# Kernel tuning notes

Measured on AMD Instinct MI355X. Metric: run time of the kernel, lower is better.

The kernel has to match this reference:

```python
import jax, jax.numpy as jnp
import numpy as np

KSZ = 3      # kernel_size
NH = 4       # num_heads


def setup_inputs() -> dict:
    key = jax.random.key(0)
    ks = jax.random.split(key, 4)
    B, D, H, W, C = 1, 28, 28, 28, 192
    N = D * H * W
    s = 0.02  # trunc_normal std used by the module's init
    return {
        "x": jax.random.normal(ks[0], (B, N, C), jnp.float32),
        "Wq": jax.random.normal(ks[1], (C, C), jnp.float32) * s,
        "bq": jnp.zeros((C,), jnp.float32),
        "Wkv": jax.random.normal(ks[2], (C, 2 * C), jnp.float32) * s,
        "bkv": jnp.zeros((2 * C,), jnp.float32),
        "Wp": jax.random.normal(ks[3], (C, C), jnp.float32) * s,
        "bp": jnp.zeros((C,), jnp.float32),
        "D": D, "H": H, "W": W,
    }


def _windows(t, D, H, W):
    # t: (B, D+2, H+2, W+2, nh, hc) zero-padded; gather the 27 neighborhood
    # offsets (same flattening order as unfold: d-major, then h, then w).
    return jnp.stack(
        [t[:, dz:dz + D, dy:dy + H, dx:dx + W]
         for dz in range(KSZ) for dy in range(KSZ) for dx in range(KSZ)],
        axis=4)  # (B, D, H, W, 27, nh, hc)


def reference(x, Wq, bq, Wkv, bkv, Wp, bp, D, H, W):
    B, N, C = x.shape
    hc = C // NH
    scale = hc ** (-0.5)
    xv = x.reshape(B, D, H, W, C)

    q = (xv @ Wq + bq).reshape(B, D, H, W, NH, hc) * scale
    kv = (xv @ Wkv + bkv).reshape(B, D, H, W, 2, NH, hc)
    k, v = kv[..., 0, :, :], kv[..., 1, :, :]

    pad = ((0, 0), (1, 1), (1, 1), (1, 1), (0, 0), (0, 0))
    kwin = _windows(jnp.pad(k, pad), D, H, W)  # (B,D,H,W,27,nh,hc)
    vwin = _windows(jnp.pad(v, pad), D, H, W)

    # per-voxel 1x27 attention over the 3x3x3 neighborhood
    attn = jnp.einsum('bdhwnc,bdhwknc->bdhwnk', q, kwin)
    attn = jax.nn.softmax(attn, axis=-1)
    out = jnp.einsum('bdhwnk,bdhwknc->bdhwnc', attn, vwin)
    out = out.reshape(B, D, H, W, C) @ Wp + bp
    return out.reshape(B, N, C)
```

## Files before the change

### kernel.cpp

```cpp
#include <hip/hip_runtime.h>
#include <hip/hip_bf16.h>
#include <math.h>

#define CDIM 192
#define DD 28
#define NVOX (DD * DD * DD)
#define NLINE (DD * DD)
#define LSTRIDE (24 * DD * 8)

typedef __attribute__((ext_vector_type(8))) short bf16x8;
typedef __attribute__((ext_vector_type(4))) float f32x4;

__device__ __forceinline__ float blo(unsigned int u) {
  union { unsigned int i; float f; } w; w.i = u << 16; return w.f;
}
__device__ __forceinline__ float bhi(unsigned int u) {
  union { unsigned int i; float f; } w; w.i = u & 0xffff0000u; return w.f;
}
__device__ __forceinline__ unsigned short f2bf(float f) {
  union { float ff; unsigned int i; } w; w.ff = f;
  unsigned int x = w.i;
  return (unsigned short)((x + 0x7fffu + ((x >> 16) & 1u)) >> 16);
}
__device__ __forceinline__ unsigned int pk2(float lo, float hi) {
  __hip_bfloat162 h = __float22bfloat162_rn(make_float2(lo, hi));
  union { __hip_bfloat162 h2; unsigned int u; } cv; cv.h2 = h; return cv.u;
}

__global__ __launch_bounds__(256) void prep_w(
    const float* __restrict__ Wq, const float* __restrict__ Wkv,
    const float* __restrict__ Wp, const float* __restrict__ bq,
    const float* __restrict__ bkv,
    unsigned short* __restrict__ WqkvT, unsigned short* __restrict__ WpT,
    float* __restrict__ biasAll, float scale)
{
  int t = blockIdx.x * 256 + threadIdx.x;
  if (t < 576 * CDIM) {
    const int n = t / CDIM, k = t % CDIM;
    const float v = (n < CDIM) ? Wq[k * CDIM + n] * scale
                               : Wkv[k * 2 * CDIM + (n - CDIM)];
    WqkvT[t] = f2bf(v);
    return;
  }
  t -= 576 * CDIM;
  if (t < CDIM * CDIM) {
    const int n = t / CDIM, k = t % CDIM;
    WpT[t] = f2bf(Wp[k * CDIM + n]);
    return;
  }
  t -= CDIM * CDIM;
  if (t < 576)
    biasAll[t] = (t < CDIM) ? bq[t] * scale : bkv[t - CDIM];
}

__global__ __launch_bounds__(256) void gemm_qkv(
    const float* __restrict__ X,
    const unsigned short* __restrict__ Bt,
    const float* __restrict__ biasAll,
    unsigned short* __restrict__ qb,
    unsigned short* __restrict__ kxb,
    unsigned short* __restrict__ vxb)
{
  __shared__ unsigned short As[64 * 200];
  __shared__ unsigned short Bs[64 * 200];
  const int tid = threadIdx.x;
  const int m0 = blockIdx.x * 64;
  const int by = blockIdx.y;

#pragma unroll
  for (int u = tid; u < 1536; u += 256) {
    const int row = u / 24, c = (u % 24) * 8;
    const float4 f0 = *(const float4*)(&X[(size_t)(m0 + row) * CDIM + c]);
    const float4 f1 = *(const float4*)(&X[(size_t)(m0 + row) * CDIM + c + 4]);
    unsigned int o[4] = {pk2(f0.x, f0.y), pk2(f0.z, f0.w),
                         pk2(f1.x, f1.y), pk2(f1.z, f1.w)};
    *(uint4*)(&As[row * 200 + c]) = *(const uint4*)o;
  }

  const int l = tid & 63, w = tid >> 6;
  const int wm = (w >> 1) * 32, wn = (w & 1) * 32;
  const int lr = l & 15, lk = (l >> 4) * 8;
  const unsigned short* pa = &As[(wm + lr) * 200 + lk];
  const unsigned short* pb = &Bs[(wn + lr) * 200 + lk];

  for (int nt = by; nt < 9; nt += 3) {
    const int n0 = nt * 64;
    __syncthreads();
#pragma unroll
    for (int u = tid; u < 1536; u += 256) {
      const int row = u / 24, c = (u % 24) * 8;
      *(uint4*)(&Bs[row * 200 + c]) =
          *(const uint4*)(&Bt[(size_t)(n0 + row) * CDIM + c]);
    }
    __syncthreads();

    f32x4 acc[2][2] = {};
#pragma unroll
    for (int k0 = 0; k0 < CDIM; k0 += 32) {
      const bf16x8 a0 = *(const bf16x8*)(pa + k0);
      const bf16x8 a1 = *(const bf16x8*)(pa + 16 * 200 + k0);
      const bf16x8 b0 = *(const bf16x8*)(pb + k0);
      const bf16x8 b1 = *(const bf16x8*)(pb + 16 * 200 + k0);
      acc[0][0] = __builtin_amdgcn_mfma_f32_16x16x32_bf16(a0, b0, acc[0][0], 0, 0, 0);
      acc[0][1] = __builtin_amdgcn_mfma_f32_16x16x32_bf16(a0, b1, acc[0][1], 0, 0, 0);
      acc[1][0] = __builtin_amdgcn_mfma_f32_16x16x32_bf16(a1, b0, acc[1][0], 0, 0, 0);
      acc[1][1] = __builtin_amdgcn_mfma_f32_16x16x32_bf16(a1, b1, acc[1][1], 0, 0, 0);
    }

#pragma unroll
    for (int i = 0; i < 2; ++i)
#pragma unroll
      for (int j = 0; j < 2; ++j) {
        const int gc = n0 + wn + j * 16 + lr;
        const float bv = biasAll[gc];
#pragma unroll
        for (int r = 0; r < 4; ++r) {
          const int gr = m0 + wm + i * 16 + (l >> 4) * 4 + r;
          const float v = acc[i][j][r] + bv;
          const unsigned short bfv = f2bf(v);
          if (gc < CDIM) {
            qb[(size_t)gr * CDIM + gc] = bfv;
          } else {
            const int cc = (gc < 2 * CDIM) ? gc - CDIM : gc - 2 * CDIM;
            const int zy = gr / DD, xx = gr - zy * DD;
            const int dst = zy * LSTRIDE + (cc >> 3) * (DD * 8) + xx * 8 + (cc & 7);
            if (gc < 2 * CDIM) kxb[dst] = bfv;
            else               vxb[dst] = bfv;
          }
        }
      }
  }
}

__global__ __launch_bounds__(256, 3) void attn3d_xint(
    const unsigned short* __restrict__ q,
    const unsigned short* __restrict__ kx,
    const unsigned short* __restrict__ vx,
    unsigned short* __restrict__ y)
{
  const int bid = blockIdx.x;
  const int zy = (bid & 7) * 98 + (bid >> 3);
  const int z = zy / 28, yr = zy % 28;
  const int h = threadIdx.x >> 6;
  const int lane = threadIdx.x & 63;
  const int x = lane & 31;
  const int xc = x < 28 ? x : 27;
  const int g = lane >> 5;
  const int cb = h * 48 + g * 24;
  const int cgb = h * 6 + g * 3;
  const int vox = zy * 28 + xc;

  float qf[24];
  {
    const uint4* qp = (const uint4*)(q + (size_t)vox * CDIM + cb);
    const uint4 a = qp[0], b = qp[1], c = qp[2];
    const unsigned int uu[12] = {a.x, a.y, a.z, a.w, b.x, b.y, b.z, b.w,
                                 c.x, c.y, c.z, c.w};
#pragma unroll
    for (int i = 0; i < 12; ++i) { qf[2*i] = blo(uu[i]); qf[2*i+1] = bhi(uu[i]); }
  }

  const int nx = 3 - (x == 0) - (x == 27);
  const int ny = 3 - (yr == 0) - (yr == 27);
  const int nz = 3 - (z == 0) - (z == 27);
  const int noob = 27 - nx * ny * nz;
  float m = noob ? 0.f : -INFINITY;
  float s = (float)noob;
  float out[24];
#pragma unroll
  for (int i = 0; i < 24; ++i) out[i] = 0.f;

  const bool okm = (x > 0), okp = (x < 27);
  const int xm = okm ? xc - 1 : 0;
  const int xp = okp ? xc + 1 : 27;

  int offm[3], offc[3], offp[3];
#pragma unroll
  for (int i = 0; i < 3; ++i) {
    const int ub = (cgb + i) * (DD * 8);
    offm[i] = ub + xm * 8; offc[i] = ub + xc * 8; offp[i] = ub + xp * 8;
  }

  for (int dz = -1; dz <= 1; ++dz) {
    const int zz = z + dz;
    if ((unsigned)zz >= 28u) continue;
    for (int dy = -1; dy <= 1; ++dy) {
      const int yv = yr + dy;
      if ((unsigned)yv >= 28u) continue;
      const size_t lbase = (size_t)(zz * 28 + yv) * LSTRIDE;
      const unsigned short* kl = kx + lbase;
      const unsigned short* vl = vx + lbase;

      const uint4 Km0 = *(const uint4*)(kl + offm[0]);
      const uint4 Km1 = *(const uint4*)(kl + offm[1]);
      const uint4 Km2 = *(const uint4*)(kl + offm[2]);
      const uint4 Kc0 = *(const uint4*)(kl + offc[0]);
      const uint4 Kc1 = *(const uint4*)(kl + offc[1]);
      const uint4 Kc2 = *(const uint4*)(kl + offc[2]);
      const uint4 Kp0 = *(const uint4*)(kl + offp[0]);
      const uint4 Kp1 = *(const uint4*)(kl + offp[1]);
      const uint4 Kp2 = *(const uint4*)(kl + offp[2]);
      const unsigned int km[12] = {Km0.x, Km0.y, Km0.z, Km0.w, Km1.x, Km1.y,
                                   Km1.z, Km1.w, Km2.x, Km2.y, Km2.z, Km2.w};
      const unsigned int kc[12] = {Kc0.x, Kc0.y, Kc0.z, Kc0.w, Kc1.x, Kc1.y,
                                   Kc1.z, Kc1.w, Kc2.x, Kc2.y, Kc2.z, Kc2.w};
      const unsigned int kp[12] = {Kp0.x, Kp0.y, Kp0.z, Kp0.w, Kp1.x, Kp1.y,
                                   Kp1.z, Kp1.w, Kp2.x, Kp2.y, Kp2.z, Kp2.w};
      float p0 = 0.f, p1 = 0.f, p2 = 0.f;
#pragma unroll
      for (int i = 0; i < 12; ++i) {
        p0 += qf[2*i] * blo(km[i]) + qf[2*i+1] * bhi(km[i]);
        p1 += qf[2*i] * blo(kc[i]) + qf[2*i+1] * bhi(kc[i]);
        p2 += qf[2*i] * blo(kp[i]) + qf[2*i+1] * bhi(kp[i]);
      }
      p0 += __shfl_xor(p0, 32);
      p1 += __shfl_xor(p1, 32);
      p2 += __shfl_xor(p2, 32);

      const uint4 Vm0 = *(const uint4*)(vl + offm[0]);
      const uint4 Vm1 = *(const uint4*)(vl + offm[1]);
      const uint4 Vm2 = *(const uint4*)(vl + offm[2]);
      const uint4 Vc0 = *(const uint4*)(vl + offc[0]);
      const uint4 Vc1 = *(const uint4*)(vl + offc[1]);
      const uint4 Vc2 = *(const uint4*)(vl + offc[2]);
      const uint4 Vp0 = *(const uint4*)(vl + offp[0]);
      const uint4 Vp1 = *(const uint4*)(vl + offp[1]);
      const uint4 Vp2 = *(const uint4*)(vl + offp[2]);

      const float l0 = okm ? p0 : -INFINITY;
      const float l2 = okp ? p2 : -INFINITY;
      const float nm = fmaxf(m, fmaxf(p1, fmaxf(l0, l2)));
      const float sc = __expf(m - nm);
      const float w0 = okm ? __expf(p0 - nm) : 0.f;
      const float w1 = __expf(p1 - nm);
      const float w2 = okp ? __expf(p2 - nm) : 0.f;
      s = s * sc + w0 + w1 + w2;
      m = nm;

      const unsigned int vm[12] = {Vm0.x, Vm0.y, Vm0.z, Vm0.w, Vm1.x, Vm1.y,
                                   Vm1.z, Vm1.w, Vm2.x, Vm2.y, Vm2.z, Vm2.w};
      const unsigned int vc[12] = {Vc0.x, Vc0.y, Vc0.z, Vc0.w, Vc1.x, Vc1.y,
                                   Vc1.z, Vc1.w, Vc2.x, Vc2.y, Vc2.z, Vc2.w};
      const unsigned int vp[12] = {Vp0.x, Vp0.y, Vp0.z, Vp0.w, Vp1.x, Vp1.y,
                                   Vp1.z, Vp1.w, Vp2.x, Vp2.y, Vp2.z, Vp2.w};
#pragma unroll
      for (int i = 0; i < 12; ++i) {
        out[2*i]   = out[2*i]   * sc + w0 * blo(vm[i]) + w1 * blo(vc[i]) + w2 * blo(vp[i]);
        out[2*i+1] = out[2*i+1] * sc + w0 * bhi(vm[i]) + w1 * bhi(vc[i]) + w2 * bhi(vp[i]);
      }
    }
  }

  if (x < 28) {
    const float inv = 1.f / s;
    unsigned int ou[12];
#pragma unroll
    for (int i = 0; i < 12; ++i)
      ou[i] = pk2(out[2*i] * inv, out[2*i+1] * inv);
    uint4* yp = (uint4*)(y + (size_t)vox * CDIM + cb);
    yp[0] = make_uint4(ou[0], ou[1], ou[2], ou[3]);
    yp[1] = make_uint4(ou[4], ou[5], ou[6], ou[7]);
    yp[2] = make_uint4(ou[8], ou[9], ou[10], ou[11]);
  }
}

__global__ __launch_bounds__(256) void gemm_out(
    const unsigned short* __restrict__ A,
    const unsigned short* __restrict__ Bt,
    const float* __restrict__ bias,
    float* __restrict__ C)
{
  __shared__ unsigned short As[64 * 200];
  __shared__ unsigned short Bs[64 * 200];
  const int tid = threadIdx.x;
  const int n0 = blockIdx.x * 64;
  const int m0 = blockIdx.y * 64;

#pragma unroll
  for (int u = tid; u < 1536; u += 256) {
    const int row = u / 24, c = (u % 24) * 8;
    *(uint4*)(&As[row * 200 + c]) =
        *(const uint4*)(&A[(size_t)(m0 + row) * CDIM + c]);
    *(uint4*)(&Bs[row * 200 + c]) =
        *(const uint4*)(&Bt[(size_t)(n0 + row) * CDIM + c]);
  }
  __syncthreads();

  const int l = tid & 63, w = tid >> 6;
  const int wm = (w >> 1) * 32, wn = (w & 1) * 32;
  const int lr = l & 15, lk = (l >> 4) * 8;

  f32x4 acc[2][2] = {};
  const unsigned short* pa = &As[(wm + lr) * 200 + lk];
  const unsigned short* pb = &Bs[(wn + lr) * 200 + lk];

#pragma unroll
  for (int k0 = 0; k0 < CDIM; k0 += 32) {
    const bf16x8 a0 = *(const bf16x8*)(pa + k0);
    const bf16x8 a1 = *(const bf16x8*)(pa + 16 * 200 + k0);
    const bf16x8 b0 = *(const bf16x8*)(pb + k0);
    const bf16x8 b1 = *(const bf16x8*)(pb + 16 * 200 + k0);
    acc[0][0] = __builtin_amdgcn_mfma_f32_16x16x32_bf16(a0, b0, acc[0][0], 0, 0, 0);
    acc[0][1] = __builtin_amdgcn_mfma_f32_16x16x32_bf16(a0, b1, acc[0][1], 0, 0, 0);
    acc[1][0] = __builtin_amdgcn_mfma_f32_16x16x32_bf16(a1, b0, acc[1][0], 0, 0, 0);
    acc[1][1] = __builtin_amdgcn_mfma_f32_16x16x32_bf16(a1, b1, acc[1][1], 0, 0, 0);
  }

#pragma unroll
  for (int i = 0; i < 2; ++i)
#pragma unroll
    for (int j = 0; j < 2; ++j) {
      const int gc = n0 + wn + j * 16 + lr;
      const float bv = bias[gc];
#pragma unroll
      for (int r = 0; r < 4; ++r) {
        const int gr = m0 + wm + i * 16 + (l >> 4) * 4 + r;
        C[(size_t)gr * CDIM + gc] = acc[i][j][r] + bv;
      }
    }
}

extern "C" void kernel_launch(void* const* d_in, const int* in_sizes, int n_in,
                              void* d_out, int out_size, void* d_ws, size_t ws_size,
                              hipStream_t stream) {
  const float* x   = (const float*)d_in[0];
  const float* Wq  = (const float*)d_in[1];
  const float* bq  = (const float*)d_in[2];
  const float* Wkv = (const float*)d_in[3];
  const float* bkv = (const float*)d_in[4];
  const float* Wp  = (const float*)d_in[5];
  const float* bp  = (const float*)d_in[6];
  float* out = (float*)d_out;

  unsigned short* WqkvT = (unsigned short*)d_ws;
  unsigned short* WpT   = WqkvT + 576 * CDIM;
  float*          biasA = (float*)(WpT + CDIM * CDIM);
  unsigned short* qb    = (unsigned short*)(biasA + 576);
  unsigned short* kxb   = qb + (size_t)NVOX * CDIM;
  unsigned short* vxb   = kxb + (size_t)NLINE * LSTRIDE;
  unsigned short* yb    = vxb + (size_t)NLINE * LSTRIDE;

  const float scale = 1.0f / sqrtf(48.0f);

  prep_w<<<(148032 + 255) / 256, 256, 0, stream>>>(
      Wq, Wkv, Wp, bq, bkv, WqkvT, WpT, biasA, scale);

  gemm_qkv<<<dim3(NVOX / 64, 3), 256, 0, stream>>>(x, WqkvT, biasA, qb, kxb, vxb);
  attn3d_xint<<<NLINE, 256, 0, stream>>>(qb, kxb, vxb, yb);
  gemm_out<<<dim3(3, NVOX / 64), 256, 0, stream>>>(yb, WpT, bp, out);
}
```

Baseline: 146.8 us.

## Fuse output projection GEMM into attention kernel via shared-memory tile

```diff
diff --git a/kernel.cpp b/kernel.cpp
--- a/kernel.cpp
+++ b/kernel.cpp
@@ -132,12 +132,16 @@
   }
 }
 
-__global__ __launch_bounds__(256, 3) void attn3d_xint(
+__global__ __launch_bounds__(256, 3) void attn3d_proj(
     const unsigned short* __restrict__ q,
     const unsigned short* __restrict__ kx,
     const unsigned short* __restrict__ vx,
-    unsigned short* __restrict__ y)
+    const unsigned short* __restrict__ WpT,
+    const float* __restrict__ bp,
+    float* __restrict__ C)
 {
+  __shared__ unsigned short ytile[32 * 200];
+
   const int bid = blockIdx.x;
   const int zy = (bid & 7) * 98 + (bid >> 3);
   const int z = zy / 28, yr = zy % 28;
@@ -149,6 +153,9 @@
   const int cb = h * 48 + g * 24;
   const int cgb = h * 6 + g * 3;
   const int vox = zy * 28 + xc;
+
+  if (threadIdx.x < 100)
+    *(uint4*)(&ytile[28 * 200 + threadIdx.x * 8]) = make_uint4(0, 0, 0, 0);
 
   float qf[24];
   {
@@ -257,67 +264,44 @@
 #pragma unroll
     for (int i = 0; i < 12; ++i)
       ou[i] = pk2(out[2*i] * inv, out[2*i+1] * inv);
-    uint4* yp = (uint4*)(y + (size_t)vox * CDIM + cb);
+    uint4* yp = (uint4*)(&ytile[xc * 200 + cb]);
     yp[0] = make_uint4(ou[0], ou[1], ou[2], ou[3]);
     yp[1] = make_uint4(ou[4], ou[5], ou[6], ou[7]);
     yp[2] = make_uint4(ou[8], ou[9], ou[10], ou[11]);
   }
-}
-
-__global__ __launch_bounds__(256) void gemm_out(
-    const unsigned short* __restrict__ A,
-    const unsigned short* __restrict__ Bt,
-    const float* __restrict__ bias,
-    float* __restrict__ C)
-{
-  __shared__ unsigned short As[64 * 200];
-  __shared__ unsigned short Bs[64 * 200];
-  const int tid = threadIdx.x;
-  const int n0 = blockIdx.x * 64;
-  const int m0 = blockIdx.y * 64;
-
-#pragma unroll
-  for (int u = tid; u < 1536; u += 256) {
-    const int row = u / 24, c = (u % 24) * 8;
-    *(uint4*)(&As[row * 200 + c]) =
-        *(const uint4*)(&A[(size_t)(m0 + row) * CDIM + c]);
-    *(uint4*)(&Bs[row * 200 + c]) =
-        *(const uint4*)(&Bt[(size_t)(n0 + row) * CDIM + c]);
-  }
   __syncthreads();
 
-  const int l = tid & 63, w = tid >> 6;
-  const int wm = (w >> 1) * 32, wn = (w & 1) * 32;
-  const int lr = l & 15, lk = (l >> 4) * 8;
-
-  f32x4 acc[2][2] = {};
-  const unsigned short* pa = &As[(wm + lr) * 200 + lk];
-  const unsigned short* pb = &Bs[(wn + lr) * 200 + lk];
-
+  const int w = threadIdx.x >> 6;
+  const int lr = lane & 15, lk = (lane >> 4) * 8;
+  const int nb = w * 48;
+
+  f32x4 acc[2][3] = {};
 #pragma unroll
   for (int k0 = 0; k0 < CDIM; k0 += 32) {
-    const bf16x8 a0 = *(const bf16x8*)(pa + k0);
-    const bf16x8 a1 = *(const bf16x8*)(pa + 16 * 200 + k0);
-    const bf16x8 b0 = *(const bf16x8*)(pb + k0);
-    const bf16x8 b1 = *(const bf16x8*)(pb + 16 * 200 + k0);
-    acc[0][0] = __builtin_amdgcn_mfma_f32_16x16x32_bf16(a0, b0, acc[0][0], 0, 0, 0);
-    acc[0][1] = __builtin_amdgcn_mfma_f32_16x16x32_bf16(a0, b1, acc[0][1], 0, 0, 0);
-    acc[1][0] = __builtin_amdgcn_mfma_f32_16x16x32_bf16(a1, b0, acc[1][0], 0, 0, 0);
-    acc[1][1] = __builtin_amdgcn_mfma_f32_16x16x32_bf16(a1, b1, acc[1][1], 0, 0, 0);
-  }
-
-#pragma unroll
-  for (int i = 0; i < 2; ++i)
-#pragma unroll
-    for (int j = 0; j < 2; ++j) {
-      const int gc = n0 + wn + j * 16 + lr;
-      const float bv = bias[gc];
+    const bf16x8 a0 = *(const bf16x8*)(&ytile[(0 + lr) * 200 + lk + k0]);
+    const bf16x8 a1 = *(const bf16x8*)(&ytile[(16 + lr) * 200 + lk + k0]);
+#pragma unroll
+    for (int nj = 0; nj < 3; ++nj) {
+      const bf16x8 b = *(const bf16x8*)(
+          &WpT[(size_t)(nb + nj * 16 + lr) * CDIM + lk + k0]);
+      acc[0][nj] = __builtin_amdgcn_mfma_f32_16x16x32_bf16(a0, b, acc[0][nj], 0, 0, 0);
+      acc[1][nj] = __builtin_amdgcn_mfma_f32_16x16x32_bf16(a1, b, acc[1][nj], 0, 0, 0);
+    }
+  }
+
+#pragma unroll
+  for (int nj = 0; nj < 3; ++nj) {
+    const int gc = nb + nj * 16 + lr;
+    const float bv = bp[gc];
+#pragma unroll
+    for (int mi = 0; mi < 2; ++mi)
 #pragma unroll
       for (int r = 0; r < 4; ++r) {
-        const int gr = m0 + wm + i * 16 + (l >> 4) * 4 + r;
-        C[(size_t)gr * CDIM + gc] = acc[i][j][r] + bv;
+        const int row = mi * 16 + (lane >> 4) * 4 + r;
+        if (row < 28)
+          C[(size_t)(zy * 28 + row) * CDIM + gc] = acc[mi][nj][r] + bv;
       }
-    }
+  }
 }
 
 extern "C" void kernel_launch(void* const* d_in, const int* in_sizes, int n_in,
@@ -338,7 +322,6 @@
   unsigned short* qb    = (unsigned short*)(biasA + 576);
   unsigned short* kxb   = qb + (size_t)NVOX * CDIM;
   unsigned short* vxb   = kxb + (size_t)NLINE * LSTRIDE;
-  unsigned short* yb    = vxb + (size_t)NLINE * LSTRIDE;
 
   const float scale = 1.0f / sqrtf(48.0f);
 
@@ -346,6 +329,5 @@
       Wq, Wkv, Wp, bq, bkv, WqkvT, WpT, biasA, scale);
 
   gemm_qkv<<<dim3(NVOX / 64, 3), 256, 0, stream>>>(x, WqkvT, biasA, qb, kxb, vxb);
-  attn3d_xint<<<NLINE, 256, 0, stream>>>(qb, kxb, vxb, yb);
-  gemm_out<<<dim3(3, NVOX / 64), 256, 0, stream>>>(yb, WpT, bp, out);
-}
+  attn3d_proj<<<NLINE, 256, 0, stream>>>(qb, kxb, vxb, WpT, bp, out);
+}
```

Result: no change. 144.6 us (-1.5%).
